# Performance work log

Measured on AMD Instinct MI355X. Metric: run time of the kernel, lower is better.

## Reference

```python
import jax, jax.numpy as jnp
import numpy as np

D = 256      # msa channel dim
DP = 128     # pair channel dim
H = 8        # heads
DH = 32      # dim_head
INNER = H * DH  # == D
EPS = 1e-5


def _ln(x, g, b):
    mu = jnp.mean(x, axis=-1, keepdims=True)
    var = jnp.mean(jnp.square(x - mu), axis=-1, keepdims=True)
    return (x - mu) * jax.lax.rsqrt(var + EPS) * g + b


def _heads(t, n, h=H, dh=DH):
    # [B, n, H*DH] -> [B, H, n, DH]
    return t.reshape(t.shape[0], n, h, dh).transpose(0, 2, 1, 3)


def _forward(x, pair_bias, ln1_g, ln1_b, wq_w, wkv_w, wout_w, wout_b,
             hq_w, hkv_w, hout_w, hout_b, pn_g, pn_b, pl_w,
             ln2_g, ln2_b, ff_w1, ff_b1, ff_w2, ff_b2):
    b, r, l, d = x.shape  # b == 1
    scale = DH ** -0.5
    xn = _ln(x, ln1_g, ln1_b)[0]  # [R, L, D]

    # ---- width attention: over MSA rows, one attention per column ----
    wx = xn.transpose(1, 0, 2)  # [L, R, D]
    q = _heads(wx @ wq_w, r)
    kv = wx @ wkv_w
    k = _heads(kv[..., :INNER], r)
    v = _heads(kv[..., INNER:], r)
    dots = jnp.einsum('bhid,bhjd->bhij', q, k) * scale  # [L, H, R, R]
    attn = jax.nn.softmax(dots, axis=-1)
    wo = jnp.einsum('bhij,bhjd->bhid', attn, v)
    wo = wo.transpose(0, 2, 1, 3).reshape(l, r, INNER) @ wout_w + wout_b  # [L, R, D]
    w_out = wo.transpose(1, 0, 2)  # [R, L, D]  (permute(0,2,1,3) with b=1)

    # ---- height attention: over columns, tied across rows, + pair bias ----
    hx = xn  # [R, L, D]
    q = _heads(hx @ hq_w, l)               # [R, H, L, DH]
    kv = hx @ hkv_w
    k = _heads(kv[..., :INNER], l)
    v = _heads(kv[..., INNER:], l)
    # tied: sum over rows r, extra r^-0.5 scaling
    dots = jnp.einsum('rhid,rhjd->hij', q, k) * scale * (r ** -0.5)  # [H, L, L]
    bias = jnp.einsum('ijp,ph->hij', _ln(pair_bias[0], pn_g, pn_b), pl_w)
    attn = jax.nn.softmax(dots + bias, axis=-1)  # [H, L, L]
    ho = jnp.einsum('hij,rhjd->rhid', attn, v)   # [R, H, L, DH]
    ho = ho.transpose(0, 2, 1, 3).reshape(r, l, INNER) @ hout_w + hout_b  # [R, L, D]

    x = x + ((w_out + ho) / 2)[None]

    # ---- feedforward with residual ----
    xn2 = _ln(x, ln2_g, ln2_b)
    ff = jax.nn.relu(xn2 @ ff_w1 + ff_b1) @ ff_w2 + ff_b2
    return x + ff


def setup_inputs() -> dict:
    key = jax.random.key(0)
    ks = jax.random.split(key, 24)
    rn = lambda k, shape, s=0.02: (jax.random.normal(k, shape, jnp.float32) * s)
    R, L = 128, 384
    return {
        'x': jax.random.normal(ks[0], (1, R, L, D), jnp.float32),
        'pair_bias': jax.random.normal(ks[1], (1, L, L, DP), jnp.float32),
        'ln1_g': jnp.ones((D,), jnp.float32), 'ln1_b': jnp.zeros((D,), jnp.float32),
        'wq_w': rn(ks[2], (D, INNER)), 'wkv_w': rn(ks[3], (D, 2 * INNER)),
        'wout_w': rn(ks[4], (INNER, D)), 'wout_b': jnp.zeros((D,), jnp.float32),
        'hq_w': rn(ks[5], (D, INNER)), 'hkv_w': rn(ks[6], (D, 2 * INNER)),
        'hout_w': rn(ks[7], (INNER, D)), 'hout_b': jnp.zeros((D,), jnp.float32),
        'pn_g': jnp.ones((DP,), jnp.float32), 'pn_b': jnp.zeros((DP,), jnp.float32),
        'pl_w': rn(ks[8], (DP, H)),
        'ln2_g': jnp.ones((D,), jnp.float32), 'ln2_b': jnp.zeros((D,), jnp.float32),
        'ff_w1': rn(ks[9], (D, 4 * D)), 'ff_b1': jnp.zeros((4 * D,), jnp.float32),
        'ff_w2': rn(ks[10], (4 * D, D)), 'ff_b2': jnp.zeros((D,), jnp.float32),
    }


def reference(x, pair_bias, ln1_g, ln1_b, wq_w, wkv_w, wout_w, wout_b,
              hq_w, hkv_w, hout_w, hout_b, pn_g, pn_b, pl_w,
              ln2_g, ln2_b, ff_w1, ff_b1, ff_w2, ff_b2):
    return _forward(x, pair_bias, ln1_g, ln1_b, wq_w, wkv_w, wout_w, wout_b,
                    hq_w, hkv_w, hout_w, hout_b, pn_g, pn_b, pl_w,
                    ln2_g, ln2_b, ff_w1, ff_b1, ff_w2, ff_b2)
```

## Files before the change

### kernel.cpp

```cpp
#include <hip/hip_runtime.h>

typedef float f32x4 __attribute__((ext_vector_type(4)));
typedef short bf16x8v __attribute__((ext_vector_type(8)));
typedef unsigned short u16;
typedef unsigned int u32;

#define DEVI static __device__ __forceinline__

constexpr int R_ = 128, L_ = 384, D_ = 256, H_ = 8;
constexpr int RL_ = R_ * L_;

constexpr size_t A_OFF = 0;
constexpr size_t B_OFF = 25165824;
constexpr size_t C_OFF = 100663296;
constexpr size_t D_OFF = 125829120;
constexpr size_t F_OFF = 130547712;
constexpr size_t EW_W    = 132907008;
constexpr size_t EW_H    = 133300224;
constexpr size_t EW_WOUT = 133693440;
constexpr size_t EW_HOUT = 133824512;
constexpr size_t EW_FF1  = 133955584;
constexpr size_t EW_FF2  = 134479872;
constexpr size_t EW_WP   = 135004160;
constexpr size_t EW_WC   = 135008256;

DEVI u16 f2bf(float f) {
  unsigned int b = __builtin_bit_cast(unsigned int, f);
  b += 0x7FFFu + ((b >> 16) & 1u);
  return (u16)(b >> 16);
}

#define MFMA16(a, b, c) __builtin_amdgcn_mfma_f32_16x16x32_bf16(a, b, c, 0, 0, 0)

typedef __attribute__((address_space(3))) u32 lds_u32;
typedef const __attribute__((address_space(1))) u32 glb_u32;
DEVI void gld16(const void* g, void* l) {
  __builtin_amdgcn_global_load_lds((glb_u32*)g, (lds_u32*)l, 16, 0, 0);
}

__global__ void transp_kernel(const float* __restrict__ src, u16* __restrict__ dst,
                              int K, int N) {
  int idx = blockIdx.x * 256 + threadIdx.x;
  if (idx >= K * N) return;
  int k = idx / N, n = idx - k * N;
  dst[(size_t)n * K + k] = f2bf(src[idx]);
}

__global__ void pairprep_kernel(const float* __restrict__ png, const float* __restrict__ pnb,
                                const float* __restrict__ plw,
                                float* __restrict__ wprime, float* __restrict__ wc) {
  int p = threadIdx.x;
  if (p < 128) {
    float g = png[p];
    #pragma unroll
    for (int h = 0; h < 8; ++h) wprime[p * 8 + h] = g * plw[p * 8 + h];
  }
  if (threadIdx.x == 0) {
    for (int h = 0; h < 8; ++h) {
      float W = 0.f, C = 0.f;
      for (int q = 0; q < 128; ++q) { W += png[q] * plw[q * 8 + h]; C += pnb[q] * plw[q * 8 + h]; }
      wc[h] = W; wc[8 + h] = C;
    }
  }
}

DEVI void ln_store(float4 v, const float* __restrict__ g, const float* __restrict__ b,
                   u16* __restrict__ dst, int lane) {
  float s1 = v.x + v.y + v.z + v.w;
  float s2 = v.x * v.x + v.y * v.y + v.z * v.z + v.w * v.w;
  #pragma unroll
  for (int off = 1; off < 64; off <<= 1) { s1 += __shfl_xor(s1, off); s2 += __shfl_xor(s2, off); }
  float mu = s1 * (1.f / 256.f);
  float rstd = rsqrtf(s2 * (1.f / 256.f) - mu * mu + 1e-5f);
  float4 gg = *(const float4*)(g + lane * 4);
  float4 bb = *(const float4*)(b + lane * 4);
  ushort4 o = make_ushort4(f2bf((v.x - mu) * rstd * gg.x + bb.x),
                           f2bf((v.y - mu) * rstd * gg.y + bb.y),
                           f2bf((v.z - mu) * rstd * gg.z + bb.z),
                           f2bf((v.w - mu) * rstd * gg.w + bb.w));
  *(ushort4*)dst = o;
}

__global__ __launch_bounds__(256) void ln1_kernel(const float* __restrict__ x,
                                                  const float* __restrict__ g,
                                                  const float* __restrict__ b,
                                                  u16* __restrict__ out) {
  int wid = (blockIdx.x * 256 + threadIdx.x) >> 6;
  if (wid >= RL_) return;
  int lane = threadIdx.x & 63;
  float4 v = *(const float4*)(x + (size_t)wid * 256 + lane * 4);
  ln_store(v, g, b, out + (size_t)wid * 256 + lane * 4, lane);
}

__global__ __launch_bounds__(256) void resln_kernel(const float* __restrict__ x,
                                                    float* __restrict__ io,
                                                    const float* __restrict__ g,
                                                    const float* __restrict__ b,
                                                    u16* __restrict__ out) {
  int wid = (blockIdx.x * 256 + threadIdx.x) >> 6;
  if (wid >= RL_) return;
  int lane = threadIdx.x & 63;
  size_t base = (size_t)wid * 256 + lane * 4;
  float4 xv = *(const float4*)(x + base);
  float4 ov = *(const float4*)(io + base);
  float4 nv = make_float4(xv.x + 0.5f * ov.x, xv.y + 0.5f * ov.y,
                          xv.z + 0.5f * ov.z, xv.w + 0.5f * ov.w);
  *(float4*)(io + base) = nv;
  ln_store(nv, g, b, out + base, lane);
}

__global__ __launch_bounds__(256) void gemm128_kernel(
    const u16* __restrict__ A, const u16* __restrict__ B, void* __restrict__ Cv,
    const float* __restrict__ bias,
    int M, int N, int K,
    int lda, long long kasb, int ldbn, long long kbsb, int ldc, long long cnsb,
    long long abase, long long bbase, long long cbase,
    int Z2, long long as1, long long as2, long long bs1, long long bs2,
    long long cs1, long long cs2,
    float alpha, int flags) {
  __shared__ __align__(16) u16 SM[16384];
  int z = blockIdx.z, z1 = z / Z2, z2 = z - z1 * Z2;
  long long aoff = abase + z1 * as1 + z2 * as2;
  long long boff = bbase + z1 * bs1 + z2 * bs2;
  long long coff = cbase + z1 * cs1 + z2 * cs2;
  int m0 = blockIdx.x * 128, n0 = blockIdx.y * 128;
  int tid = threadIdx.x, lane = tid & 63, w = tid >> 6;
  int wm = w >> 1, wn = w & 1;

  const u16* pA[2]; const u16* pB[2];
  #pragma unroll
  for (int q = 0; q < 2; ++q) {
    int row = (w * 2 + q) * 16 + (lane >> 2);
    int g = (lane & 3) ^ ((row >> 1) & 3);
    pA[q] = A + aoff + (long long)(m0 + row) * lda + g * 8;
    pB[q] = B + boff + (long long)(n0 + row) * ldbn + g * 8;
  }

  f32x4 acc[4][4] = {};
  int nkt = K >> 5;

  #pragma unroll
  for (int q = 0; q < 2; ++q) {
    gld16(pA[q], &SM[(w * 2 + q) * 512]);
    gld16(pB[q], &SM[8192 + (w * 2 + q) * 512]);
  }

  for (int t = 0; t < nkt; ++t) {
    int cur = t & 1;
    const u16* aC = &SM[cur * 4096];
    const u16* bC = &SM[8192 + cur * 4096];
    if (t + 1 < nkt) {
      long long ta = (long long)(t + 1) * kasb;
      long long tb = (long long)(t + 1) * kbsb;
      #pragma unroll
      for (int q = 0; q < 2; ++q) {
        gld16(pA[q] + ta, &SM[(cur ^ 1) * 4096 + (w * 2 + q) * 512]);
        gld16(pB[q] + tb, &SM[8192 + (cur ^ 1) * 4096 + (w * 2 + q) * 512]);
      }
      asm volatile("s_waitcnt vmcnt(4)" ::: "memory");
    } else {
      asm volatile("s_waitcnt vmcnt(0)" ::: "memory");
    }
    __builtin_amdgcn_sched_barrier(0);
    __builtin_amdgcn_s_barrier();
    __builtin_amdgcn_sched_barrier(0);
    bf16x8v af[4], bf[4];
    #pragma unroll
    for (int f = 0; f < 4; ++f) {
      int rowA = wm * 64 + f * 16 + (lane & 15);
      int cA = (lane >> 4) ^ ((rowA >> 1) & 3);
      af[f] = *(const bf16x8v*)&aC[rowA * 32 + cA * 8];
      int rowB = wn * 64 + f * 16 + (lane & 15);
      int cB = (lane >> 4) ^ ((rowB >> 1) & 3);
      bf[f] = *(const bf16x8v*)&bC[rowB * 32 + cB * 8];
    }
    __builtin_amdgcn_s_setprio(1);
    #pragma unroll
    for (int mt = 0; mt < 4; ++mt)
      #pragma unroll
      for (int nt = 0; nt < 4; ++nt)
        acc[mt][nt] = MFMA16(af[mt], bf[nt], acc[mt][nt]);
    __builtin_amdgcn_s_setprio(0);
    __builtin_amdgcn_sched_barrier(0);
    __builtin_amdgcn_s_barrier();
  }

  bool obf = flags & 1, beta = flags & 2, relu = flags & 4, atom = flags & 8;
  float* Cf = (float*)Cv;
  u16* Cb = (u16*)Cv;
  if (obf) {
    u16* Cs = SM;
    #pragma unroll
    for (int mt = 0; mt < 4; ++mt)
      #pragma unroll
      for (int nt = 0; nt < 4; ++nt)
        #pragma unroll
        for (int rg = 0; rg < 4; ++rg) {
          int m = wm * 64 + mt * 16 + (lane >> 4) * 4 + rg;
          int n = wn * 64 + nt * 16 + (lane & 15);
          float v = alpha * acc[mt][nt][rg];
          if (bias) v += bias[n0 + n];
          if (relu) v = fmaxf(v, 0.f);
          Cs[m * 128 + n] = f2bf(v);
        }
    __builtin_amdgcn_s_barrier();
    #pragma unroll
    for (int q = 0; q < 8; ++q) {
      int slot = q * 256 + tid;
      int m = slot >> 4, ns = (slot & 15) * 8;
      int ng = n0 + ns;
      long long ci = coff + (long long)(m0 + m) * ldc + (long long)(ng >> 5) * cnsb + (ng & 31);
      *(uint4*)(Cb + ci) = *(const uint4*)&Cs[m * 128 + ns];
    }
  } else {
    #pragma unroll
    for (int mt = 0; mt < 4; ++mt)
      #pragma unroll
      for (int nt = 0; nt < 4; ++nt)
        #pragma unroll
        for (int rg = 0; rg < 4; ++rg) {
          int m = m0 + wm * 64 + mt * 16 + (lane >> 4) * 4 + rg;
          int n = n0 + wn * 64 + nt * 16 + (lane & 15);
          float v = alpha * acc[mt][nt][rg];
          if (bias) v += bias[n];
          long long ci = coff + (long long)m * ldc + (long long)(n >> 5) * cnsb + (n & 31);
          if (atom) {
            atomicAdd(&Cf[ci], v);
          } else {
            if (beta) v += Cf[ci];
            if (relu) v = fmaxf(v, 0.f);
            Cf[ci] = v;
          }
        }
  }
}

__global__ __launch_bounds__(768, 3) void ffn_kernel(
    const u16* __restrict__ xn2,
    const u16* __restrict__ w1t,
    const float* __restrict__ b1,
    const u16* __restrict__ w2t,
    const float* __restrict__ b2,
    float* __restrict__ io) {
  __shared__ __align__(16) u16 W1c[2][8192];
  __shared__ __align__(16) u16 W2c[2][8192];
  __shared__ __align__(16) u16 HSa[12 * 640];
  int tid = threadIdx.x, lane = tid & 63, w = tid >> 6;
  int m0 = blockIdx.x * 192 + w * 16;

  bf16x8v af[8];
  #pragma unroll
  for (int ksl = 0; ksl < 8; ++ksl)
    af[ksl] = *(const bf16x8v*)(xn2 + (size_t)(m0 + (lane & 15)) * 256 + ksl * 32 + (lane >> 4) * 8);

  u16* HS = HSa + w * 640;
  f32x4 acc2[16] = {};

  auto STAGE = [&](int c, int d) {
    if (w < 8) {
      #pragma unroll
      for (int q = 0; q < 4; ++q) {
        int o = w * 4 + q;
        if (o < 16) {
          int r = o * 2 + (lane >> 5);
          int g = lane & 31;
          int gs = (g & 24) | ((g & 7) ^ (r & 7));
          gld16(w1t + (size_t)(c * 32 + r) * 256 + gs * 8, &W1c[d][o * 512]);
        } else {
          int o2 = o - 16;
          int r = o2 * 16 + (lane >> 2);
          int gs = (lane & 3) ^ ((r >> 1) & 3);
          gld16(w2t + (size_t)r * 1024 + c * 32 + gs * 8, &W2c[d][o2 * 512]);
        }
      }
    }
  };

  STAGE(0, 0);
  __syncthreads();

  #pragma unroll 1
  for (int c = 0; c < 32; ++c) {
    int cur = c & 1;
    if (c + 1 < 32) {
      STAGE(c + 1, cur ^ 1);
      asm volatile("s_waitcnt vmcnt(4)" ::: "memory");
    } else {
      asm volatile("s_waitcnt vmcnt(0)" ::: "memory");
    }
    __builtin_amdgcn_sched_barrier(0);
    __builtin_amdgcn_s_barrier();
    __builtin_amdgcn_sched_barrier(0);

    f32x4 acc1[2] = {};
    #pragma unroll
    for (int ks = 0; ks < 8; ++ks) {
      #pragma unroll
      for (int nf = 0; nf < 2; ++nf) {
        int row = nf * 16 + (lane & 15);
        int cg = ks * 4 + (lane >> 4);
        int ch = (cg & 24) | ((cg & 7) ^ (row & 7));
        bf16x8v bf = *(const bf16x8v*)&W1c[cur][row * 256 + ch * 8];
        acc1[nf] = MFMA16(af[ks], bf, acc1[nf]);
      }
    }
    #pragma unroll
    for (int nf = 0; nf < 2; ++nf) {
      int col = nf * 16 + (lane & 15);
      float bias = b1[c * 32 + col];
      #pragma unroll
      for (int rg = 0; rg < 4; ++rg) {
        float v = fmaxf(acc1[nf][rg] + bias, 0.f);
        HS[((lane >> 4) * 4 + rg) * 40 + col] = f2bf(v);
      }
    }
    bf16x8v ahs = *(const bf16x8v*)&HS[(lane & 15) * 40 + (lane >> 4) * 8];
    __builtin_amdgcn_s_setprio(1);
    #pragma unroll
    for (int nf = 0; nf < 16; ++nf) {
      int n2 = nf * 16 + (lane & 15);
      int ch = (lane >> 4) ^ ((n2 >> 1) & 3);
      bf16x8v bf = *(const bf16x8v*)&W2c[cur][n2 * 32 + ch * 8];
      acc2[nf] = MFMA16(ahs, bf, acc2[nf]);
    }
    __builtin_amdgcn_s_setprio(0);
    __builtin_amdgcn_sched_barrier(0);
    __builtin_amdgcn_s_barrier();
  }

  #pragma unroll
  for (int nf = 0; nf < 16; ++nf) {
    int n = nf * 16 + (lane & 15);
    float bb = b2[n];
    #pragma unroll
    for (int rg = 0; rg < 4; ++rg) {
      int row = m0 + (lane >> 4) * 4 + rg;
      size_t ci = (size_t)row * 256 + n;
      io[ci] += acc2[nf][rg] + bb;
    }
  }
}

__global__ __launch_bounds__(256) void wattn_kernel(const u16* __restrict__ proj,
                                                    u16* __restrict__ outc) {
  int l = blockIdx.x >> 3, h = blockIdx.x & 7;
  int tid = threadIdx.x, lane = tid & 63, w = tid >> 6;
  __shared__ u16 Pl[128][136];
  __shared__ u16 Vl[128][40];
  {
    int r = tid >> 1, dh0 = (tid & 1) * 16;
    const u16* src = proj + ((size_t)(r * L_ + l)) * 768 + 512 + h * 32 + dh0;
    *(uint4*)&Vl[r][dh0] = *(const uint4*)src;
    *(uint4*)&Vl[r][dh0 + 8] = *(const uint4*)(src + 8);
  }
  f32x4 s[2][8] = {};
  bf16x8v qf[2];
  #pragma unroll
  for (int mt = 0; mt < 2; ++mt) {
    int row = w * 32 + mt * 16 + (lane & 15);
    qf[mt] = *(const bf16x8v*)(proj + ((size_t)(row * L_ + l)) * 768 + h * 32 + (lane >> 4) * 8);
  }
  #pragma unroll
  for (int ct = 0; ct < 8; ++ct) {
    int col = ct * 16 + (lane & 15);
    bf16x8v kf = *(const bf16x8v*)(proj + ((size_t)(col * L_ + l)) * 768 + 256 + h * 32 + (lane >> 4) * 8);
    s[0][ct] = MFMA16(qf[0], kf, s[0][ct]);
    s[1][ct] = MFMA16(qf[1], kf, s[1][ct]);
  }
  const float scale = 0.1767766952966369f;
  #pragma unroll
  for (int mt = 0; mt < 2; ++mt)
    #pragma unroll
    for (int rg = 0; rg < 4; ++rg) {
      float mx = -1e30f;
      #pragma unroll
      for (int ct = 0; ct < 8; ++ct) { s[mt][ct][rg] *= scale; mx = fmaxf(mx, s[mt][ct][rg]); }
      #pragma unroll
      for (int off = 1; off < 16; off <<= 1) mx = fmaxf(mx, __shfl_xor(mx, off));
      float sum = 0.f;
      #pragma unroll
      for (int ct = 0; ct < 8; ++ct) { float pv = __expf(s[mt][ct][rg] - mx); s[mt][ct][rg] = pv; sum += pv; }
      #pragma unroll
      for (int off = 1; off < 16; off <<= 1) sum += __shfl_xor(sum, off);
      float inv = 1.f / sum;
      int row = w * 32 + mt * 16 + (lane >> 4) * 4 + rg;
      #pragma unroll
      for (int ct = 0; ct < 8; ++ct) Pl[row][ct * 16 + (lane & 15)] = f2bf(s[mt][ct][rg] * inv);
    }
  __syncthreads();
  f32x4 o[2][2] = {};
  #pragma unroll
  for (int kk = 0; kk < 4; ++kk) {
    bf16x8v pa[2];
    #pragma unroll
    for (int mt = 0; mt < 2; ++mt)
      pa[mt] = *(const bf16x8v*)&Pl[w * 32 + mt * 16 + (lane & 15)][kk * 32 + (lane >> 4) * 8];
    #pragma unroll
    for (int nt = 0; nt < 2; ++nt) {
      bf16x8v vb;
      #pragma unroll
      for (int e = 0; e < 8; ++e) vb[e] = (short)Vl[kk * 32 + (lane >> 4) * 8 + e][nt * 16 + (lane & 15)];
      o[0][nt] = MFMA16(pa[0], vb, o[0][nt]);
      o[1][nt] = MFMA16(pa[1], vb, o[1][nt]);
    }
  }
  #pragma unroll
  for (int mt = 0; mt < 2; ++mt)
    #pragma unroll
    for (int nt = 0; nt < 2; ++nt)
      #pragma unroll
      for (int rg = 0; rg < 4; ++rg) {
        int row = w * 32 + mt * 16 + (lane >> 4) * 4 + rg;
        int dh = nt * 16 + (lane & 15);
        outc[((size_t)(row * L_ + l)) * 256 + h * 32 + dh] = f2bf(o[mt][nt][rg]);
      }
}

__global__ __launch_bounds__(512) void pairsm_kernel(const float* __restrict__ pair,
                                                     const float* __restrict__ wprime,
                                                     const float* __restrict__ wc,
                                                     const float* __restrict__ dots,
                                                     u16* __restrict__ attn) {
  int i = blockIdx.x;
  int tid = threadIdx.x, lane = tid & 63, w = tid >> 6;
  __shared__ float bias_s[384][9];
  int sub = lane & 15, g = lane >> 4;

  float4 wv[16];
  #pragma unroll
  for (int c = 0; c < 8; ++c) {
    wv[c * 2]     = *(const float4*)(wprime + (sub * 8 + c) * 8);
    wv[c * 2 + 1] = *(const float4*)(wprime + (sub * 8 + c) * 8 + 4);
  }

  #pragma unroll 1
  for (int pass = 0; pass < 12; ++pass) {
    int j = pass * 32 + w * 4 + g;
    const float* px = pair + ((size_t)i * L_ + j) * 128 + sub * 8;
    float4 a = *(const float4*)px;
    float4 b = *(const float4*)(px + 4);
    float xa[8] = {a.x, a.y, a.z, a.w, b.x, b.y, b.z, b.w};
    float s1 = 0.f, s2 = 0.f;
    float t0 = 0, t1 = 0, t2 = 0, t3 = 0, t4 = 0, t5 = 0, t6 = 0, t7 = 0;
    #pragma unroll
    for (int c = 0; c < 8; ++c) {
      float xv = xa[c];
      s1 += xv; s2 += xv * xv;
      t0 += wv[c * 2].x * xv; t1 += wv[c * 2].y * xv;
      t2 += wv[c * 2].z * xv; t3 += wv[c * 2].w * xv;
      t4 += wv[c * 2 + 1].x * xv; t5 += wv[c * 2 + 1].y * xv;
      t6 += wv[c * 2 + 1].z * xv; t7 += wv[c * 2 + 1].w * xv;
    }
    #pragma unroll
    for (int off = 1; off < 16; off <<= 1) {
      s1 += __shfl_xor(s1, off); s2 += __shfl_xor(s2, off);
      t0 += __shfl_xor(t0, off); t1 += __shfl_xor(t1, off);
      t2 += __shfl_xor(t2, off); t3 += __shfl_xor(t3, off);
      t4 += __shfl_xor(t4, off); t5 += __shfl_xor(t5, off);
      t6 += __shfl_xor(t6, off); t7 += __shfl_xor(t7, off);
    }
    if (sub < 8) {
      float mu = s1 * (1.f / 128.f);
      float rstd = rsqrtf(s2 * (1.f / 128.f) - mu * mu + 1e-5f);
      float tv = t0;
      if (sub == 1) tv = t1; if (sub == 2) tv = t2; if (sub == 3) tv = t3;
      if (sub == 4) tv = t4; if (sub == 5) tv = t5; if (sub == 6) tv = t6;
      if (sub == 7) tv = t7;
      bias_s[j][sub] = rstd * (tv - mu * wc[sub]) + wc[8 + sub];
    }
  }
  __syncthreads();

  int h = w;
  const float* dr = dots + ((size_t)h * L_ + i) * L_;
  float v[6];
  #pragma unroll
  for (int u = 0; u < 6; ++u) v[u] = dr[lane + u * 64] + bias_s[lane + u * 64][h];
  float mx = v[0];
  #pragma unroll
  for (int u = 1; u < 6; ++u) mx = fmaxf(mx, v[u]);
  #pragma unroll
  for (int off = 1; off < 64; off <<= 1) mx = fmaxf(mx, __shfl_xor(mx, off));
  float s = 0.f;
  #pragma unroll
  for (int u = 0; u < 6; ++u) { v[u] = __expf(v[u] - mx); s += v[u]; }
  #pragma unroll
  for (int off = 1; off < 64; off <<= 1) s += __shfl_xor(s, off);
  float inv = 1.f / s;
  #pragma unroll
  for (int u = 0; u < 6; ++u)
    attn[((size_t)h * L_ + i) * L_ + lane + u * 64] = f2bf(v[u] * inv);
}

__global__ __launch_bounds__(256) void vt_kernel(const u16* __restrict__ proj,
                                                 u16* __restrict__ vt) {
  int bz = blockIdx.x;
  int jc = bz % 6, hr = bz / 6;
  int h = hr >> 7, r = hr & 127;
  int j0 = jc * 64;
  __shared__ u16 T[64][40];
  int t = threadIdx.x;
  {
    int jr = t >> 2, seg = t & 3;
    *(uint4*)&T[jr][seg * 8] =
        *(const uint4*)(proj + ((size_t)(r * L_ + j0 + jr)) * 768 + 512 + h * 32 + seg * 8);
  }
  __syncthreads();
  {
    int dr = t >> 3, sg = t & 7;
    u16 tmp[8];
    #pragma unroll
    for (int u = 0; u < 8; ++u) tmp[u] = T[sg * 8 + u][dr];
    uint4 pk;
    pk.x = (unsigned)tmp[0] | ((unsigned)tmp[1] << 16);
    pk.y = (unsigned)tmp[2] | ((unsigned)tmp[3] << 16);
    pk.z = (unsigned)tmp[4] | ((unsigned)tmp[5] << 16);
    pk.w = (unsigned)tmp[6] | ((unsigned)tmp[7] << 16);
    *(uint4*)(vt + ((size_t)hr * 32 + dr) * 384 + j0 + sg * 8) = pk;
  }
}

extern "C" void kernel_launch(void* const* d_in, const int* in_sizes, int n_in,
                              void* d_out, int out_size, void* d_ws, size_t ws_size,
                              hipStream_t stream) {
  const float* x      = (const float*)d_in[0];
  const float* pair   = (const float*)d_in[1];
  const float* ln1_g  = (const float*)d_in[2];
  const float* ln1_b  = (const float*)d_in[3];
  const float* wq_w   = (const float*)d_in[4];
  const float* wkv_w  = (const float*)d_in[5];
  const float* wout_w = (const float*)d_in[6];
  const float* wout_b = (const float*)d_in[7];
  const float* hq_w   = (const float*)d_in[8];
  const float* hkv_w  = (const float*)d_in[9];
  const float* hout_w = (const float*)d_in[10];
  const float* hout_b = (const float*)d_in[11];
  const float* pn_g   = (const float*)d_in[12];
  const float* pn_b   = (const float*)d_in[13];
  const float* pl_w   = (const float*)d_in[14];
  const float* ln2_g  = (const float*)d_in[15];
  const float* ln2_b  = (const float*)d_in[16];
  const float* ff_w1  = (const float*)d_in[17];
  const float* ff_b1  = (const float*)d_in[18];
  const float* ff_w2  = (const float*)d_in[19];
  const float* ff_b2  = (const float*)d_in[20];

  char* ws = (char*)d_ws;
  u16* xnA   = (u16*)(ws + A_OFF);
  u16* projB = (u16*)(ws + B_OFF);
  u16* attC  = (u16*)(ws + C_OFF);
  float* dotsD = (float*)(ws + D_OFF);
  u16* attnF = (u16*)(ws + F_OFF);
  u16* wqkvT_w = (u16*)(ws + EW_W);
  u16* wqkvT_h = (u16*)(ws + EW_H);
  u16* woutT = (u16*)(ws + EW_WOUT);
  u16* houtT = (u16*)(ws + EW_HOUT);
  u16* ff1T  = (u16*)(ws + EW_FF1);
  u16* ff2T  = (u16*)(ws + EW_FF2);
  float* wprime = (float*)(ws + EW_WP);
  float* wc     = (float*)(ws + EW_WC);
  float* outF = (float*)d_out;

  transp_kernel<<<dim3(256), dim3(256), 0, stream>>>(wq_w, wqkvT_w, 256, 256);
  transp_kernel<<<dim3(512), dim3(256), 0, stream>>>(wkv_w, wqkvT_w + 256 * 256, 256, 512);
  transp_kernel<<<dim3(256), dim3(256), 0, stream>>>(hq_w, wqkvT_h, 256, 256);
  transp_kernel<<<dim3(512), dim3(256), 0, stream>>>(hkv_w, wqkvT_h + 256 * 256, 256, 512);
  transp_kernel<<<dim3(256), dim3(256), 0, stream>>>(wout_w, woutT, 256, 256);
  transp_kernel<<<dim3(256), dim3(256), 0, stream>>>(hout_w, houtT, 256, 256);
  transp_kernel<<<dim3(1024), dim3(256), 0, stream>>>(ff_w1, ff1T, 256, 1024);
  transp_kernel<<<dim3(1024), dim3(256), 0, stream>>>(ff_w2, ff2T, 1024, 256);
  pairprep_kernel<<<dim3(1), dim3(128), 0, stream>>>(pn_g, pn_b, pl_w, wprime, wc);

  hipMemsetAsync(dotsD, 0, (size_t)H_ * L_ * L_ * 4, stream);

  ln1_kernel<<<dim3(RL_ / 4), dim3(256), 0, stream>>>(x, ln1_g, ln1_b, xnA);

  gemm128_kernel<<<dim3(384, 6, 1), dim3(256), 0, stream>>>(
      xnA, wqkvT_w, projB, nullptr, RL_, 768, 256,
      256, 32LL, 256, 32LL, 768, 32LL, 0LL, 0LL, 0LL,
      1, 0LL, 0LL, 0LL, 0LL, 0LL, 0LL, 1.f, 1 );

  wattn_kernel<<<dim3(L_ * H_), dim3(256), 0, stream>>>(projB, attC);

  gemm128_kernel<<<dim3(384, 2, 1), dim3(256), 0, stream>>>(
      attC, woutT, outF, wout_b, RL_, 256, 256,
      256, 32LL, 256, 32LL, 256, 32LL, 0LL, 0LL, 0LL,
      1, 0LL, 0LL, 0LL, 0LL, 0LL, 0LL, 1.f, 0);

  gemm128_kernel<<<dim3(384, 6, 1), dim3(256), 0, stream>>>(
      xnA, wqkvT_h, projB, nullptr, RL_, 768, 256,
      256, 32LL, 256, 32LL, 768, 32LL, 0LL, 0LL, 0LL,
      1, 0LL, 0LL, 0LL, 0LL, 0LL, 0LL, 1.f, 1);

  gemm128_kernel<<<dim3(3, 3, 32), dim3(256), 0, stream>>>(
      projB, projB, dotsD, nullptr, 384, 384, 1024,
      768, (long long)L_ * 768, 768, (long long)L_ * 768, 384, 32LL,
      0LL, 256LL, 0LL,
      4, 32LL, 32LL * L_ * 768, 32LL, 32LL * L_ * 768,
      (long long)L_ * L_, 0LL, 1.f / 64.f, 8 );

  pairsm_kernel<<<dim3(L_), dim3(512), 0, stream>>>(pair, wprime, wc, dotsD, attnF);

  vt_kernel<<<dim3(H_ * R_ * 6), dim3(256), 0, stream>>>(projB, xnA);

  gemm128_kernel<<<dim3(3, 32, 8), dim3(256), 0, stream>>>(
      attnF, xnA, attC, nullptr, 384, 4096, 384,
      384, 32LL, 384, 32LL, 256, (long long)L_ * 256,
      0LL, 0LL, 0LL,
      8, 0LL, (long long)L_ * L_, 0LL, 1572864LL, 0LL, 32LL, 1.f, 1 );

  gemm128_kernel<<<dim3(384, 2, 1), dim3(256), 0, stream>>>(
      attC, houtT, outF, hout_b, RL_, 256, 256,
      256, 32LL, 256, 32LL, 256, 32LL, 0LL, 0LL, 0LL,
      1, 0LL, 0LL, 0LL, 0LL, 0LL, 0LL, 1.f, 2 );

  resln_kernel<<<dim3(RL_ / 4), dim3(256), 0, stream>>>(x, outF, ln2_g, ln2_b, xnA);

  ffn_kernel<<<dim3(256), dim3(768), 0, stream>>>(
      xnA, ff1T, ff_b1, ff2T, ff_b2, outF);
}
```

Baseline: 488.0 us.

## Restructure FFN kernel to 3 waves each computing 32 rows

The fused FFN kernel drops from 12 waves of 16 rows per block to 3 waves of 32 rows each, with 512 blocks of 96 rows. Each wave now reuses every W1/W2 fragment read from LDS for two row tiles, which halves LDS weight traffic per MFMA. All waves now share the weight staging and the wait count is raised to match. The cost is roughly double the accumulator registers per wave, fewer waves per block to hide latency, and 1-wave-per-SIMD launch bounds.

```diff
diff --git a/kernel.cpp b/kernel.cpp
--- a/kernel.cpp
+++ b/kernel.cpp
@@ -235,7 +235,7 @@
   }
 }
 
-__global__ __launch_bounds__(768, 3) void ffn_kernel(
+__global__ __launch_bounds__(192, 1) void ffn_kernel(
     const u16* __restrict__ xn2,
     const u16* __restrict__ w1t,
     const float* __restrict__ b1,
@@ -244,23 +244,26 @@
     float* __restrict__ io) {
   __shared__ __align__(16) u16 W1c[2][8192];
   __shared__ __align__(16) u16 W2c[2][8192];
-  __shared__ __align__(16) u16 HSa[12 * 640];
+  __shared__ __align__(16) u16 HSa[3 * 1280];
   int tid = threadIdx.x, lane = tid & 63, w = tid >> 6;
-  int m0 = blockIdx.x * 192 + w * 16;
-
-  bf16x8v af[8];
-  #pragma unroll
-  for (int ksl = 0; ksl < 8; ++ksl)
-    af[ksl] = *(const bf16x8v*)(xn2 + (size_t)(m0 + (lane & 15)) * 256 + ksl * 32 + (lane >> 4) * 8);
-
-  u16* HS = HSa + w * 640;
-  f32x4 acc2[16] = {};
+  int m0 = blockIdx.x * 96 + w * 32;
+
+  bf16x8v af2[2][8];
+  #pragma unroll
+  for (int rt = 0; rt < 2; ++rt)
+    #pragma unroll
+    for (int ks = 0; ks < 8; ++ks)
+      af2[rt][ks] = *(const bf16x8v*)(xn2 + (size_t)(m0 + rt * 16 + (lane & 15)) * 256 +
+                                      ks * 32 + (lane >> 4) * 8);
+
+  u16* HS = HSa + w * 1280;
+  f32x4 acc2[2][16] = {};
 
   auto STAGE = [&](int c, int d) {
-    if (w < 8) {
-      #pragma unroll
-      for (int q = 0; q < 4; ++q) {
-        int o = w * 4 + q;
+    #pragma unroll
+    for (int oi = 0; oi < 11; ++oi) {
+      int o = w + oi * 3;
+      if (o < 32) {
         if (o < 16) {
           int r = o * 2 + (lane >> 5);
           int g = lane & 31;
@@ -277,6 +280,7 @@
   };
 
   STAGE(0, 0);
+  asm volatile("s_waitcnt vmcnt(0)" ::: "memory");
   __syncthreads();
 
   #pragma unroll 1
@@ -284,7 +288,7 @@
     int cur = c & 1;
     if (c + 1 < 32) {
       STAGE(c + 1, cur ^ 1);
-      asm volatile("s_waitcnt vmcnt(4)" ::: "memory");
+      asm volatile("s_waitcnt vmcnt(10)" ::: "memory");
     } else {
       asm volatile("s_waitcnt vmcnt(0)" ::: "memory");
     }
@@ -292,7 +296,7 @@
     __builtin_amdgcn_s_barrier();
     __builtin_amdgcn_sched_barrier(0);
 
-    f32x4 acc1[2] = {};
+    f32x4 acc1[2][2] = {};
     #pragma unroll
     for (int ks = 0; ks < 8; ++ks) {
       #pragma unroll
@@ -301,27 +305,35 @@
         int cg = ks * 4 + (lane >> 4);
         int ch = (cg & 24) | ((cg & 7) ^ (row & 7));
         bf16x8v bf = *(const bf16x8v*)&W1c[cur][row * 256 + ch * 8];
-        acc1[nf] = MFMA16(af[ks], bf, acc1[nf]);
+        acc1[0][nf] = MFMA16(af2[0][ks], bf, acc1[0][nf]);
+        acc1[1][nf] = MFMA16(af2[1][ks], bf, acc1[1][nf]);
       }
     }
+    int q = lane >> 4;
     #pragma unroll
     for (int nf = 0; nf < 2; ++nf) {
       int col = nf * 16 + (lane & 15);
       float bias = b1[c * 32 + col];
       #pragma unroll
-      for (int rg = 0; rg < 4; ++rg) {
-        float v = fmaxf(acc1[nf][rg] + bias, 0.f);
-        HS[((lane >> 4) * 4 + rg) * 40 + col] = f2bf(v);
-      }
-    }
-    bf16x8v ahs = *(const bf16x8v*)&HS[(lane & 15) * 40 + (lane >> 4) * 8];
+      for (int rt = 0; rt < 2; ++rt)
+        #pragma unroll
+        for (int rg = 0; rg < 4; ++rg) {
+          float v = fmaxf(acc1[rt][nf][rg] + bias, 0.f);
+          HS[(rt * 16 + q * 4 + rg) * 40 + col] = f2bf(v);
+        }
+    }
+    bf16x8v ahs[2];
+    #pragma unroll
+    for (int rt = 0; rt < 2; ++rt)
+      ahs[rt] = *(const bf16x8v*)&HS[(rt * 16 + (lane & 15)) * 40 + (lane >> 4) * 8];
     __builtin_amdgcn_s_setprio(1);
     #pragma unroll
     for (int nf = 0; nf < 16; ++nf) {
       int n2 = nf * 16 + (lane & 15);
       int ch = (lane >> 4) ^ ((n2 >> 1) & 3);
       bf16x8v bf = *(const bf16x8v*)&W2c[cur][n2 * 32 + ch * 8];
-      acc2[nf] = MFMA16(ahs, bf, acc2[nf]);
+      acc2[0][nf] = MFMA16(ahs[0], bf, acc2[0][nf]);
+      acc2[1][nf] = MFMA16(ahs[1], bf, acc2[1][nf]);
     }
     __builtin_amdgcn_s_setprio(0);
     __builtin_amdgcn_sched_barrier(0);
@@ -329,16 +341,18 @@
   }
 
   #pragma unroll
-  for (int nf = 0; nf < 16; ++nf) {
-    int n = nf * 16 + (lane & 15);
-    float bb = b2[n];
-    #pragma unroll
-    for (int rg = 0; rg < 4; ++rg) {
-      int row = m0 + (lane >> 4) * 4 + rg;
-      size_t ci = (size_t)row * 256 + n;
-      io[ci] += acc2[nf][rg] + bb;
-    }
-  }
+  for (int rt = 0; rt < 2; ++rt)
+    #pragma unroll
+    for (int nf = 0; nf < 16; ++nf) {
+      int n = nf * 16 + (lane & 15);
+      float bb = b2[n];
+      #pragma unroll
+      for (int rg = 0; rg < 4; ++rg) {
+        int row = m0 + rt * 16 + (lane >> 4) * 4 + rg;
+        size_t ci = (size_t)row * 256 + n;
+        io[ci] += acc2[rt][nf][rg] + bb;
+      }
+    }
 }
 
 __global__ __launch_bounds__(256) void wattn_kernel(const u16* __restrict__ proj,
@@ -616,6 +630,6 @@
 
   resln_kernel<<<dim3(RL_ / 4), dim3(256), 0, stream>>>(x, outF, ln2_g, ln2_b, xnA);
 
-  ffn_kernel<<<dim3(256), dim3(768), 0, stream>>>(
+  ffn_kernel<<<dim3(512), dim3(192), 0, stream>>>(
       xnA, ff1T, ff_b1, ff2T, ff_b2, outF);
 }
```

Result: slower. 584.5 us (+19.8%).

## Fuse width and height output projections into one K-concatenated GEMM

Applied to the files above, without the earlier changes.

Replaces the two separate output-projection GEMMs (width then height, each K=256 writing and accumulating into the output) with one GEMM over K=512. The A operand switches from the width-attention buffer to the height-attention buffer at a k-split point, and the B operand is a concatenated transposed weight. The summed biases are precomputed. This removes one full read-modify-write pass over the fp32 output and one launch. The cost is a per-tile branch in the load path, an extra pointer set, and reuse of workspace regions (projB and the wqkv weights) that relies on their earlier contents no longer being needed.

```diff
diff --git a/kernel.cpp b/kernel.cpp
--- a/kernel.cpp
+++ b/kernel.cpp
@@ -23,6 +23,7 @@
 constexpr size_t EW_FF2  = 134479872;
 constexpr size_t EW_WP   = 135004160;
 constexpr size_t EW_WC   = 135008256;
+constexpr size_t EW_BS   = 135008320;
 
 DEVI u16 f2bf(float f) {
   unsigned int b = __builtin_bit_cast(unsigned int, f);
@@ -39,21 +40,25 @@
 }
 
 __global__ void transp_kernel(const float* __restrict__ src, u16* __restrict__ dst,
-                              int K, int N) {
+                              int K, int N, int dstK, int koff) {
   int idx = blockIdx.x * 256 + threadIdx.x;
   if (idx >= K * N) return;
   int k = idx / N, n = idx - k * N;
-  dst[(size_t)n * K + k] = f2bf(src[idx]);
+  dst[(size_t)n * dstK + koff + k] = f2bf(src[idx]);
 }
 
 __global__ void pairprep_kernel(const float* __restrict__ png, const float* __restrict__ pnb,
                                 const float* __restrict__ plw,
-                                float* __restrict__ wprime, float* __restrict__ wc) {
+                                const float* __restrict__ woutb, const float* __restrict__ houtb,
+                                float* __restrict__ wprime, float* __restrict__ wc,
+                                float* __restrict__ bsum) {
   int p = threadIdx.x;
   if (p < 128) {
     float g = png[p];
     #pragma unroll
     for (int h = 0; h < 8; ++h) wprime[p * 8 + h] = g * plw[p * 8 + h];
+    bsum[p] = woutb[p] + houtb[p];
+    bsum[p + 128] = woutb[p + 128] + houtb[p + 128];
   }
   if (threadIdx.x == 0) {
     for (int h = 0; h < 8; ++h) {
@@ -110,11 +115,11 @@
 }
 
 __global__ __launch_bounds__(256) void gemm128_kernel(
-    const u16* __restrict__ A, const u16* __restrict__ B, void* __restrict__ Cv,
-    const float* __restrict__ bias,
+    const u16* __restrict__ A, const u16* __restrict__ A2, const u16* __restrict__ B,
+    void* __restrict__ Cv, const float* __restrict__ bias,
     int M, int N, int K,
     int lda, long long kasb, int ldbn, long long kbsb, int ldc, long long cnsb,
-    long long abase, long long bbase, long long cbase,
+    long long abase, long long bbase, long long cbase, int ksplit,
     int Z2, long long as1, long long as2, long long bs1, long long bs2,
     long long cs1, long long cs2,
     float alpha, int flags) {
@@ -127,13 +132,14 @@
   int tid = threadIdx.x, lane = tid & 63, w = tid >> 6;
   int wm = w >> 1, wn = w & 1;
 
-  const u16* pA[2]; const u16* pB[2];
+  const u16* pA[2]; const u16* pA2[2]; const u16* pB[2];
   #pragma unroll
   for (int q = 0; q < 2; ++q) {
     int row = (w * 2 + q) * 16 + (lane >> 2);
     int g = (lane & 3) ^ ((row >> 1) & 3);
-    pA[q] = A + aoff + (long long)(m0 + row) * lda + g * 8;
-    pB[q] = B + boff + (long long)(n0 + row) * ldbn + g * 8;
+    pA[q]  = A  + aoff + (long long)(m0 + row) * lda + g * 8;
+    pA2[q] = A2 + aoff + (long long)(m0 + row) * lda + g * 8;
+    pB[q]  = B  + boff + (long long)(n0 + row) * ldbn + g * 8;
   }
 
   f32x4 acc[4][4] = {};
@@ -150,12 +156,13 @@
     const u16* aC = &SM[cur * 4096];
     const u16* bC = &SM[8192 + cur * 4096];
     if (t + 1 < nkt) {
-      long long ta = (long long)(t + 1) * kasb;
-      long long tb = (long long)(t + 1) * kbsb;
+      int tn = t + 1;
       #pragma unroll
       for (int q = 0; q < 2; ++q) {
-        gld16(pA[q] + ta, &SM[(cur ^ 1) * 4096 + (w * 2 + q) * 512]);
-        gld16(pB[q] + tb, &SM[8192 + (cur ^ 1) * 4096 + (w * 2 + q) * 512]);
+        const u16* srcA = (tn < ksplit) ? (pA[q] + (long long)tn * kasb)
+                                        : (pA2[q] + (long long)(tn - ksplit) * kasb);
+        gld16(srcA, &SM[(cur ^ 1) * 4096 + (w * 2 + q) * 512]);
+        gld16(pB[q] + (long long)tn * kbsb, &SM[8192 + (cur ^ 1) * 4096 + (w * 2 + q) * 512]);
       }
       asm volatile("s_waitcnt vmcnt(4)" ::: "memory");
     } else {
@@ -548,54 +555,53 @@
   char* ws = (char*)d_ws;
   u16* xnA   = (u16*)(ws + A_OFF);
   u16* projB = (u16*)(ws + B_OFF);
+  u16* hattB = (u16*)(ws + B_OFF);
   u16* attC  = (u16*)(ws + C_OFF);
   float* dotsD = (float*)(ws + D_OFF);
   u16* attnF = (u16*)(ws + F_OFF);
   u16* wqkvT_w = (u16*)(ws + EW_W);
+  u16* oT      = (u16*)(ws + EW_W);
   u16* wqkvT_h = (u16*)(ws + EW_H);
-  u16* woutT = (u16*)(ws + EW_WOUT);
-  u16* houtT = (u16*)(ws + EW_HOUT);
   u16* ff1T  = (u16*)(ws + EW_FF1);
   u16* ff2T  = (u16*)(ws + EW_FF2);
   float* wprime = (float*)(ws + EW_WP);
   float* wc     = (float*)(ws + EW_WC);
+  float* bsum   = (float*)(ws + EW_BS);
   float* outF = (float*)d_out;
-
-  transp_kernel<<<dim3(256), dim3(256), 0, stream>>>(wq_w, wqkvT_w, 256, 256);
-  transp_kernel<<<dim3(512), dim3(256), 0, stream>>>(wkv_w, wqkvT_w + 256 * 256, 256, 512);
-  transp_kernel<<<dim3(256), dim3(256), 0, stream>>>(hq_w, wqkvT_h, 256, 256);
-  transp_kernel<<<dim3(512), dim3(256), 0, stream>>>(hkv_w, wqkvT_h + 256 * 256, 256, 512);
-  transp_kernel<<<dim3(256), dim3(256), 0, stream>>>(wout_w, woutT, 256, 256);
-  transp_kernel<<<dim3(256), dim3(256), 0, stream>>>(hout_w, houtT, 256, 256);
-  transp_kernel<<<dim3(1024), dim3(256), 0, stream>>>(ff_w1, ff1T, 256, 1024);
-  transp_kernel<<<dim3(1024), dim3(256), 0, stream>>>(ff_w2, ff2T, 1024, 256);
-  pairprep_kernel<<<dim3(1), dim3(128), 0, stream>>>(pn_g, pn_b, pl_w, wprime, wc);
+  constexpr int KBIG = 1 << 30;
+
+  transp_kernel<<<dim3(256), dim3(256), 0, stream>>>(wq_w, wqkvT_w, 256, 256, 256, 0);
+  transp_kernel<<<dim3(512), dim3(256), 0, stream>>>(wkv_w, wqkvT_w + 256 * 256, 256, 512, 256, 0);
+  transp_kernel<<<dim3(256), dim3(256), 0, stream>>>(hq_w, wqkvT_h, 256, 256, 256, 0);
+  transp_kernel<<<dim3(512), dim3(256), 0, stream>>>(hkv_w, wqkvT_h + 256 * 256, 256, 512, 256, 0);
+  transp_kernel<<<dim3(1024), dim3(256), 0, stream>>>(ff_w1, ff1T, 256, 1024, 256, 0);
+  transp_kernel<<<dim3(1024), dim3(256), 0, stream>>>(ff_w2, ff2T, 1024, 256, 1024, 0);
+  pairprep_kernel<<<dim3(1), dim3(128), 0, stream>>>(pn_g, pn_b, pl_w, wout_b, hout_b,
+                                                     wprime, wc, bsum);
 
   hipMemsetAsync(dotsD, 0, (size_t)H_ * L_ * L_ * 4, stream);
 
   ln1_kernel<<<dim3(RL_ / 4), dim3(256), 0, stream>>>(x, ln1_g, ln1_b, xnA);
 
   gemm128_kernel<<<dim3(384, 6, 1), dim3(256), 0, stream>>>(
-      xnA, wqkvT_w, projB, nullptr, RL_, 768, 256,
-      256, 32LL, 256, 32LL, 768, 32LL, 0LL, 0LL, 0LL,
+      xnA, xnA, wqkvT_w, projB, nullptr, RL_, 768, 256,
+      256, 32LL, 256, 32LL, 768, 32LL, 0LL, 0LL, 0LL, KBIG,
       1, 0LL, 0LL, 0LL, 0LL, 0LL, 0LL, 1.f, 1 );
 
+  transp_kernel<<<dim3(256), dim3(256), 0, stream>>>(wout_w, oT, 256, 256, 512, 0);
+  transp_kernel<<<dim3(256), dim3(256), 0, stream>>>(hout_w, oT, 256, 256, 512, 256);
+
   wattn_kernel<<<dim3(L_ * H_), dim3(256), 0, stream>>>(projB, attC);
 
-  gemm128_kernel<<<dim3(384, 2, 1), dim3(256), 0, stream>>>(
-      attC, woutT, outF, wout_b, RL_, 256, 256,
-      256, 32LL, 256, 32LL, 256, 32LL, 0LL, 0LL, 0LL,
-      1, 0LL, 0LL, 0LL, 0LL, 0LL, 0LL, 1.f, 0);
-
   gemm128_kernel<<<dim3(384, 6, 1), dim3(256), 0, stream>>>(
-      xnA, wqkvT_h, projB, nullptr, RL_, 768, 256,
-      256, 32LL, 256, 32LL, 768, 32LL, 0LL, 0LL, 0LL,
+      xnA, xnA, wqkvT_h, projB, nullptr, RL_, 768, 256,
+      256, 32LL, 256, 32LL, 768, 32LL, 0LL, 0LL, 0LL, KBIG,
       1, 0LL, 0LL, 0LL, 0LL, 0LL, 0LL, 1.f, 1);
 
   gemm128_kernel<<<dim3(3, 3, 32), dim3(256), 0, stream>>>(
-      projB, projB, dotsD, nullptr, 384, 384, 1024,
+      projB, projB, projB, dotsD, nullptr, 384, 384, 1024,
       768, (long long)L_ * 768, 768, (long long)L_ * 768, 384, 32LL,
-      0LL, 256LL, 0LL,
+      0LL, 256LL, 0LL, KBIG,
       4, 32LL, 32LL * L_ * 768, 32LL, 32LL * L_ * 768,
       (long long)L_ * L_, 0LL, 1.f / 64.f, 8 );
 
@@ -604,15 +610,15 @@
   vt_kernel<<<dim3(H_ * R_ * 6), dim3(256), 0, stream>>>(projB, xnA);
 
   gemm128_kernel<<<dim3(3, 32, 8), dim3(256), 0, stream>>>(
-      attnF, xnA, attC, nullptr, 384, 4096, 384,
+      attnF, attnF, xnA, hattB, nullptr, 384, 4096, 384,
       384, 32LL, 384, 32LL, 256, (long long)L_ * 256,
-      0LL, 0LL, 0LL,
+      0LL, 0LL, 0LL, KBIG,
       8, 0LL, (long long)L_ * L_, 0LL, 1572864LL, 0LL, 32LL, 1.f, 1 );
 
   gemm128_kernel<<<dim3(384, 2, 1), dim3(256), 0, stream>>>(
-      attC, houtT, outF, hout_b, RL_, 256, 256,
-      256, 32LL, 256, 32LL, 256, 32LL, 0LL, 0LL, 0LL,
-      1, 0LL, 0LL, 0LL, 0LL, 0LL, 0LL, 1.f, 2 );
+      attC, hattB, oT, outF, bsum, RL_, 256, 512,
+      256, 32LL, 512, 32LL, 256, 32LL, 0LL, 0LL, 0LL, 8 ,
+      1, 0LL, 0LL, 0LL, 0LL, 0LL, 0LL, 1.f, 0);
 
   resln_kernel<<<dim3(RL_ / 4), dim3(256), 0, stream>>>(x, outF, ln2_g, ln2_b, xnA);
 
```

Result: faster. 451.8 us (-7.4%).
